# Kernel tuning notes

Hardware: AMD Instinct MI355X
Metric: run time of the kernel (lower is better)

Reference implementation:

```python
import jax, jax.numpy as jnp
import numpy as np

N, E, G = 50000, 800000, 512
DIN, HID, DOUT, L, DE = 64, 64, 128, 3, 16
NEG_SLOPE = 0.2
BN_EPS = 1e-5


def setup_inputs() -> dict:
    key = jax.random.key(0)
    ks = jax.random.split(key, 20)
    s = 0.1  # weight scale for numerical stability
    return {
        "x": jax.random.normal(ks[0], (N, DIN), jnp.float32),
        "edge_index": jax.random.randint(ks[1], (2, E), 0, N, jnp.int32),
        "edge_attr": jax.random.normal(ks[2], (E, DE), jnp.float32),
        "batch": jnp.sort(jax.random.randint(ks[3], (N,), 0, G, jnp.int32)),
        "emb_W": jax.random.normal(ks[4], (HID, DIN), jnp.float32) * s,
        "emb_b": jax.random.normal(ks[5], (HID,), jnp.float32) * s,
        "Wl": jax.random.normal(ks[6], (L, HID, HID), jnp.float32) * s,
        "bl": jax.random.normal(ks[7], (L, HID), jnp.float32) * s,
        "Wr": jax.random.normal(ks[8], (L, HID, HID), jnp.float32) * s,
        "br": jax.random.normal(ks[9], (L, HID), jnp.float32) * s,
        "We": jax.random.normal(ks[10], (L, HID, DE), jnp.float32) * s,
        "att": jax.random.normal(ks[11], (L, HID), jnp.float32) * s,
        "conv_bias": jax.random.normal(ks[12], (L, HID), jnp.float32) * s,
        "bn_gamma": jax.random.uniform(ks[13], (L, HID), jnp.float32, 0.5, 1.5),
        "bn_beta": jax.random.normal(ks[14], (L, HID), jnp.float32) * s,
        "bn_mean": jnp.zeros((L, HID), jnp.float32),
        "bn_var": jnp.ones((L, HID), jnp.float32),
        "lin_W": jax.random.normal(ks[15], (DOUT, HID), jnp.float32) * s,
        "lin_b": jax.random.normal(ks[16], (DOUT,), jnp.float32) * s,
    }


def _gatv2(h, src, dst, edge_attr, Wl, bl, Wr, br, We, att, bias):
    # GATv2Conv, heads=1, concat=False, with edge features
    xl = h @ Wl.T + bl                      # [N,C] source transform (also message value)
    xr = h @ Wr.T + br                      # [N,C] target transform
    ea = edge_attr @ We.T                   # [E,C]
    m = xl[src] + xr[dst] + ea              # [E,C]
    m = jax.nn.leaky_relu(m, NEG_SLOPE)
    alpha = m @ att                         # [E] attention logits
    amax = jax.ops.segment_max(alpha, dst, num_segments=N)
    ea_exp = jnp.exp(alpha - amax[dst])
    denom = jax.ops.segment_sum(ea_exp, dst, num_segments=N)
    alpha = ea_exp / (denom[dst] + 1e-16)
    out = jax.ops.segment_sum(alpha[:, None] * xl[src], dst, num_segments=N)
    return out + bias


def reference(x, edge_index, edge_attr, batch, emb_W, emb_b, Wl, bl, Wr, br,
              We, att, conv_bias, bn_gamma, bn_beta, bn_mean, bn_var, lin_W, lin_b):
    src, dst = edge_index[0], edge_index[1]
    h = x @ emb_W.T + emb_b
    for i in range(L):
        hc = _gatv2(h, src, dst, edge_attr, Wl[i], bl[i], Wr[i], br[i],
                    We[i], att[i], conv_bias[i])
        # BatchNorm (eval mode, running stats)
        hc = (hc - bn_mean[i]) * jax.lax.rsqrt(bn_var[i] + BN_EPS) * bn_gamma[i] + bn_beta[i]
        hc = jax.nn.gelu(hc, approximate=False)  # torch F.gelu default is exact erf
        h = h + hc                                # residual; dropout p=0 / eval -> identity
    out = h @ lin_W.T + lin_b                     # [N,DOUT]
    counts = jax.ops.segment_sum(jnp.ones((N,), out.dtype), batch, num_segments=G)
    pooled = jax.ops.segment_sum(out, batch, num_segments=G)
    return pooled / jnp.maximum(counts, 1.0)[:, None]
```

## Files before the change

### kernel.cpp

```cpp
#include <hip/hip_runtime.h>
#include <math.h>

#define NEG_SLOPE 0.2f
#define BN_EPS 1e-5f

template <int N> struct IC { static constexpr int v = N; };
template <bool B> struct BC { static constexpr bool v = B; };

typedef _Float16 half2v __attribute__((ext_vector_type(2)));
typedef _Float16 f16x8 __attribute__((ext_vector_type(8)));
typedef float f32x4v __attribute__((ext_vector_type(4)));

__device__ __forceinline__ half2v u2h(unsigned u) {
  union { unsigned u; half2v h; } c;
  c.u = u;
  return c.h;
}
__device__ __forceinline__ unsigned pkh(float lo, float hi) {
  union { half2v h; unsigned u; } c;
  c.h[0] = (_Float16)lo;
  c.h[1] = (_Float16)hi;
  return c.u;
}

#if defined(__has_builtin)
#if __has_builtin(__builtin_amdgcn_fdot2)
#define FDOT2(a, b, c) __builtin_amdgcn_fdot2((a), (b), (c), false)
#endif
#endif
#ifndef FDOT2
__device__ __forceinline__ float fdot2_sw(half2v a, half2v b, float c) {
  return c + (float)a[0] * (float)b[0] + (float)a[1] * (float)b[1];
}
#define FDOT2(a, b, c) fdot2_sw((a), (b), (c))
#endif

#if defined(__has_builtin)
#if __has_builtin(__builtin_amdgcn_exp2f)
#define FEXP(x) __builtin_amdgcn_exp2f(x)
#define ATT_SCALE 1.44269504088896f
#endif
#endif
#ifndef FEXP
#define FEXP(x) __expf(x)
#define ATT_SCALE 1.0f
#endif

#define FMA4(acc, v, wq) \
  acc += (v).x * (wq).x + (v).y * (wq).y + (v).z * (wq).z + (v).w * (wq).w

#define DOT_ROW(buf, r, bias, OUT)                                     \
  {                                                                    \
    __builtin_amdgcn_sched_barrier(0);                                 \
    float a0 = 0.f, a1 = 0.f, a2 = 0.f, a3 = 0.f;                      \
    _Pragma("unroll") for (int q = 0; q < 4; q++) {                    \
      float4 v0 = *(const float4*)((buf) + (r) * 64 + q * 16 + 0);     \
      float4 v1 = *(const float4*)((buf) + (r) * 64 + q * 16 + 4);     \
      float4 v2 = *(const float4*)((buf) + (r) * 64 + q * 16 + 8);     \
      float4 v3 = *(const float4*)((buf) + (r) * 64 + q * 16 + 12);    \
      FMA4(a0, v0, W[q * 4 + 0]);                                      \
      FMA4(a1, v1, W[q * 4 + 1]);                                      \
      FMA4(a2, v2, W[q * 4 + 2]);                                      \
      FMA4(a3, v3, W[q * 4 + 3]);                                      \
    }                                                                  \
    OUT = (bias) + ((a0 + a1) + (a2 + a3));                            \
  }

__device__ __forceinline__ float wave_sum64(float v) {
  int x;
  x = __builtin_amdgcn_update_dpp(0, __float_as_int(v), 0x121, 0xF, 0xF, true);
  v += __int_as_float(x);
  x = __builtin_amdgcn_update_dpp(0, __float_as_int(v), 0x122, 0xF, 0xF, true);
  v += __int_as_float(x);
  x = __builtin_amdgcn_update_dpp(0, __float_as_int(v), 0x124, 0xF, 0xF, true);
  v += __int_as_float(x);
  x = __builtin_amdgcn_update_dpp(0, __float_as_int(v), 0x128, 0xF, 0xF, true);
  v += __int_as_float(x);
  x = __builtin_amdgcn_update_dpp(0, __float_as_int(v), 0x142, 0xF, 0xF, true);
  v += __int_as_float(x);
  x = __builtin_amdgcn_update_dpp(0, __float_as_int(v), 0x143, 0xF, 0xF, true);
  v += __int_as_float(x);
  return __int_as_float(__builtin_amdgcn_readlane(__float_as_int(v), 63));
}

__global__ __launch_bounds__(256) void hist_kernel(
    const int* __restrict__ dst, const int* __restrict__ batch,
    int* __restrict__ deg, float* __restrict__ counts, int E_, int N_) {
  int i = blockIdx.x * 256 + threadIdx.x;
  if (i < E_) atomicAdd(&deg[dst[i]], 1);
  if (i < N_) atomicAdd(&counts[batch[i]], 1.0f);
}

__global__ __launch_bounds__(256) void scanA_kernel(
    const int* __restrict__ deg, int* __restrict__ row_ptr,
    int* __restrict__ segTot, int N_, int nseg) {
  __shared__ int sb[256];
  int t = threadIdx.x;
  for (int s = blockIdx.x; s < nseg; s += gridDim.x) {
    int i = s * 256 + t;
    int v = (i < N_) ? deg[i] : 0;
    sb[t] = v;
    __syncthreads();
    for (int off = 1; off < 256; off <<= 1) {
      int a = (t >= off) ? sb[t - off] : 0;
      __syncthreads();
      sb[t] += a;
      __syncthreads();
    }
    int incl = sb[t];
    if (i < N_) row_ptr[i] = incl - v;
    if (t == 255) segTot[s] = incl;
    __syncthreads();
  }
}

__global__ __launch_bounds__(256) void scanB_kernel(int* __restrict__ segTot,
                                                    int nseg) {
  __shared__ int sb[256];
  __shared__ int baseSh;
  int t = threadIdx.x;
  if (t == 0) baseSh = 0;
  __syncthreads();
  for (int c0 = 0; c0 < nseg; c0 += 256) {
    int s = c0 + t;
    int v = (s < nseg) ? segTot[s] : 0;
    sb[t] = v;
    __syncthreads();
    for (int off = 1; off < 256; off <<= 1) {
      int a = (t >= off) ? sb[t - off] : 0;
      __syncthreads();
      sb[t] += a;
      __syncthreads();
    }
    int incl = sb[t];
    int base = baseSh;
    if (s < nseg) segTot[s] = base + incl - v;
    __syncthreads();
    if (t == 255) baseSh = base + incl;
    __syncthreads();
  }
}

__global__ __launch_bounds__(256) void scanC_kernel(
    int* __restrict__ row_ptr, const int* __restrict__ segTot,
    int* __restrict__ cursor, int N_, int E_) {
  int tid = blockIdx.x * 256 + threadIdx.x;
  int nt = gridDim.x * 256;
  for (int i = tid; i < N_; i += nt) {
    int rp = row_ptr[i] + segTot[i >> 8];
    row_ptr[i] = rp;
    cursor[i] = rp;
  }
  if (tid == 0) row_ptr[N_] = E_;
}

__global__ __launch_bounds__(256) void dhist_kernel(
    const int* __restrict__ row_ptr, int* __restrict__ bins, int N_) {
  __shared__ int lb[128];
  int t = threadIdx.x;
  if (t < 128) lb[t] = 0;
  __syncthreads();
  int i = blockIdx.x * 256 + t;
  if (i < N_) {
    int dg = row_ptr[i + 1] - row_ptr[i];
    atomicAdd(&lb[127 - min(dg, 127)], 1);
  }
  __syncthreads();
  if (t < 128 && lb[t]) atomicAdd(&bins[t], lb[t]);
}

__global__ __launch_bounds__(128) void dscan_kernel(int* __restrict__ bins) {
  __shared__ int sb[128];
  int t = threadIdx.x;
  int v = bins[t];
  sb[t] = v;
  __syncthreads();
  for (int off = 1; off < 128; off <<= 1) {
    int a = (t >= off) ? sb[t - off] : 0;
    __syncthreads();
    sb[t] += a;
    __syncthreads();
  }
  bins[t] = sb[t] - v;
}

__global__ __launch_bounds__(256) void dscatter_kernel(
    const int* __restrict__ row_ptr, int* __restrict__ bins,
    int* __restrict__ perm, int N_) {
  __shared__ int lb[128];
  int t = threadIdx.x;
  if (t < 128) lb[t] = 0;
  __syncthreads();
  int i = blockIdx.x * 256 + t;
  int bin = 0, r = 0;
  bool ok = (i < N_);
  if (ok) {
    int dg = row_ptr[i + 1] - row_ptr[i];
    bin = 127 - min(dg, 127);
    r = atomicAdd(&lb[bin], 1);
  }
  __syncthreads();
  if (t < 128) {
    int c = lb[t];
    lb[t] = c ? atomicAdd(&bins[t], c) : 0;
  }
  __syncthreads();
  if (ok) perm[lb[bin] + r] = i;
}

__global__ __launch_bounds__(256) void scatter_kernel(
    const int* __restrict__ src, const int* __restrict__ dst,
    int* __restrict__ cursor, int* __restrict__ csr_src,
    int* __restrict__ csr_eid, int E_) {
  int e = blockIdx.x * 256 + threadIdx.x;
  if (e >= E_) return;
  int pos = atomicAdd(&cursor[dst[e]], 1);
  csr_src[pos] = src[e];
  csr_eid[pos] = e;
}

__global__ __launch_bounds__(256) void permute_attr_kernel(
    const float4* __restrict__ edge_attr4, const int* __restrict__ csr_eid,
    unsigned* __restrict__ attr_u, int E_) {
  int p = blockIdx.x * 256 + threadIdx.x;
  if (p >= E_) return;
  int e = csr_eid[p];
  float4 a0 = edge_attr4[(size_t)e * 4 + 0];
  float4 a1 = edge_attr4[(size_t)e * 4 + 1];
  float4 a2 = edge_attr4[(size_t)e * 4 + 2];
  float4 a3 = edge_attr4[(size_t)e * 4 + 3];
  uint4 u0, u1;
  u0.x = pkh(a0.x, a0.y);
  u0.y = pkh(a0.z, a0.w);
  u0.z = pkh(a1.x, a1.y);
  u0.w = pkh(a1.z, a1.w);
  u1.x = pkh(a2.x, a2.y);
  u1.y = pkh(a2.z, a2.w);
  u1.z = pkh(a3.x, a3.y);
  u1.w = pkh(a3.z, a3.w);
  uint4* d4 = (uint4*)(attr_u + (size_t)p * 8);
  d4[0] = u0;
  d4[1] = u1;
}

__global__ __launch_bounds__(256) void pack_w16_kernel(
    const float* __restrict__ Wl, const float* __restrict__ Wr,
    _Float16* __restrict__ w16, int per) {
  int i = blockIdx.x * 256 + threadIdx.x;
  if (i < per) {
    w16[i] = (_Float16)Wl[i];
  } else if (i < 2 * per) {
    w16[i] = (_Float16)Wr[i - per];
  }
}

__global__ __launch_bounds__(256, 3) void emb_kernel(
    const float* __restrict__ x, const float* __restrict__ emb_W,
    const float* __restrict__ emb_b, float* __restrict__ h, int rows) {
  __shared__ float sx[4096];
  int lane = threadIdx.x & 63;
  int w = threadIdx.x >> 6;
  int n0 = blockIdx.x * 64;

  {
    int gmax = rows * 64 - 4;
#pragma unroll
    for (int i = 0; i < 4; i++) {
      int off = w * 1024 + i * 256 + lane * 4;
      int g = min(n0 * 64 + off, gmax);
      *(float4*)(sx + off) = *(const float4*)(x + g);
    }
  }

  float4 W[16];
#pragma unroll
  for (int q = 0; q < 16; q++) W[q] = ((const float4*)(emb_W + lane * 64))[q];
  float b = emb_b[lane];
#pragma unroll 1
  for (int t = 0; t < 16; t++) {
    int r = w * 16 + t;
    float a;
    DOT_ROW(sx, r, b, a);
    int n = n0 + r;
    if (n < rows) h[(size_t)n * 64 + lane] = a;
  }
}

#if defined(__has_builtin)
#if __has_builtin(__builtin_amdgcn_mfma_f32_16x16x32_f16)
#define HAVE_MFMA16 1
#endif
#endif

__global__ __launch_bounds__(256) void linx_mfma_kernel(
    const float* __restrict__ in, const _Float16* __restrict__ Wl16,
    const float* __restrict__ bl, const _Float16* __restrict__ Wr16,
    const float* __restrict__ br, _Float16* __restrict__ xl,
    _Float16* __restrict__ xr, int rows) {
#ifdef HAVE_MFMA16
  int lane = threadIdx.x & 63;
  int w = threadIdx.x >> 6;
  int n0 = blockIdx.x * 64 + w * 16;
  int r = lane & 15;
  int kg = lane >> 4;

  int nA = min(n0 + r, rows - 1);
  f16x8 A0, A1;
  {
    const float* p = in + (size_t)nA * 64 + kg * 8;
    float4 xa = *(const float4*)(p);
    float4 xb = *(const float4*)(p + 4);
    A0[0] = (_Float16)xa.x; A0[1] = (_Float16)xa.y;
    A0[2] = (_Float16)xa.z; A0[3] = (_Float16)xa.w;
    A0[4] = (_Float16)xb.x; A0[5] = (_Float16)xb.y;
    A0[6] = (_Float16)xb.z; A0[7] = (_Float16)xb.w;
    xa = *(const float4*)(p + 32);
    xb = *(const float4*)(p + 36);
    A1[0] = (_Float16)xa.x; A1[1] = (_Float16)xa.y;
    A1[2] = (_Float16)xa.z; A1[3] = (_Float16)xa.w;
    A1[4] = (_Float16)xb.x; A1[5] = (_Float16)xb.y;
    A1[6] = (_Float16)xb.z; A1[7] = (_Float16)xb.w;
  }

#pragma unroll
  for (int c = 0; c < 4; c++) {
    int o = c * 16 + r;
    {
      const f16x8* b0 = (const f16x8*)(Wl16 + (size_t)o * 64 + kg * 8);
      const f16x8* b1 = (const f16x8*)(Wl16 + (size_t)o * 64 + 32 + kg * 8);
      f32x4v acc;
      float bv = bl[o];
      acc[0] = bv; acc[1] = bv; acc[2] = bv; acc[3] = bv;
      acc = __builtin_amdgcn_mfma_f32_16x16x32_f16(A0, b0[0], acc, 0, 0, 0);
      acc = __builtin_amdgcn_mfma_f32_16x16x32_f16(A1, b1[0], acc, 0, 0, 0);
#pragma unroll
      for (int g = 0; g < 4; g++) {
        int nd = n0 + kg * 4 + g;
        if (nd < rows) xl[(size_t)nd * 64 + o] = (_Float16)acc[g];
      }
    }
    {
      const f16x8* b0 = (const f16x8*)(Wr16 + (size_t)o * 64 + kg * 8);
      const f16x8* b1 = (const f16x8*)(Wr16 + (size_t)o * 64 + 32 + kg * 8);
      f32x4v acc;
      float bv = br[o];
      acc[0] = bv; acc[1] = bv; acc[2] = bv; acc[3] = bv;
      acc = __builtin_amdgcn_mfma_f32_16x16x32_f16(A0, b0[0], acc, 0, 0, 0);
      acc = __builtin_amdgcn_mfma_f32_16x16x32_f16(A1, b1[0], acc, 0, 0, 0);
#pragma unroll
      for (int g = 0; g < 4; g++) {
        int nd = n0 + kg * 4 + g;
        if (nd < rows) xr[(size_t)nd * 64 + o] = (_Float16)acc[g];
      }
    }
  }
#endif
}

template <bool CONTIG>
__global__ __launch_bounds__(256) void gat_fused_kernel(
    const int* __restrict__ perm, const int* __restrict__ csr_src,
    const int* __restrict__ csr_eid, const int* __restrict__ row_ptr,
    const unsigned* __restrict__ attr_u, const float* __restrict__ edge_attr,
    const _Float16* __restrict__ xl, const _Float16* __restrict__ xr,
    const float* __restrict__ We, const float* __restrict__ att,
    const float* __restrict__ conv_bias, const float* __restrict__ gamma,
    const float* __restrict__ beta, const float* __restrict__ mean,
    const float* __restrict__ var, float* __restrict__ h, int N_) {
  int widx = (blockIdx.x * 256 + threadIdx.x) >> 6;
  if (widx >= N_) return;
  int d = __builtin_amdgcn_readfirstlane(perm[widx]);
  int j = threadIdx.x & 63;
  half2v Wek2[8];
  float Wekf[16];
  if constexpr (CONTIG) {
#pragma unroll
    for (int q = 0; q < 8; q++) {
      Wek2[q][0] = (_Float16)We[j * 16 + 2 * q];
      Wek2[q][1] = (_Float16)We[j * 16 + 2 * q + 1];
    }
  } else {
#pragma unroll
    for (int k = 0; k < 16; k++) Wekf[k] = We[j * 16 + k];
  }
  float att_j = att[j] * ATT_SCALE;
  float sc = rsqrtf(var[j] + BN_EPS) * gamma[j];
  float sh = (conv_bias[j] - mean[j]) * sc + beta[j];

  int beg = __builtin_amdgcn_readfirstlane(row_ptr[d]);
  int end = __builtin_amdgcn_readfirstlane(row_ptr[d + 1]);
  float xrj = (float)xr[(size_t)d * 64 + j];
  float m = -INFINITY, l = 0.f, acc = 0.f;

  auto chunk = [&](int base, auto C_, auto PAD_) {
    constexpr int C = decltype(C_)::v;
    constexpr bool PAD = decltype(PAD_)::v;
    int si[C];
#pragma unroll
    for (int t = 0; t < C; t++) {
      int idx = PAD ? min(base + t, end - 1) : (base + t);
      si[t] = __builtin_amdgcn_readfirstlane(csr_src[idx]);
    }
    float xlv[C];
#pragma unroll
    for (int t = 0; t < C; t++)
      xlv[t] = (float)xl[(size_t)si[t] * 64 + j];
    float v[C];
#pragma unroll
    for (int t = 0; t < C; t++) {
      int idx = PAD ? min(base + t, end - 1) : (base + t);
      float ea;
      if constexpr (CONTIG) {
        const uint4* ap = (const uint4*)(attr_u + (size_t)idx * 8);
        uint4 ua = ap[0], ub = ap[1];
        ea = 0.f;
        ea = FDOT2(u2h(ua.x), Wek2[0], ea);
        ea = FDOT2(u2h(ua.y), Wek2[1], ea);
        ea = FDOT2(u2h(ua.z), Wek2[2], ea);
        ea = FDOT2(u2h(ua.w), Wek2[3], ea);
        ea = FDOT2(u2h(ub.x), Wek2[4], ea);
        ea = FDOT2(u2h(ub.y), Wek2[5], ea);
        ea = FDOT2(u2h(ub.z), Wek2[6], ea);
        ea = FDOT2(u2h(ub.w), Wek2[7], ea);
      } else {
        const float4* ap =
            (const float4*)(edge_attr + (size_t)csr_eid[idx] * 16);
        float4 a0 = ap[0], a1 = ap[1], a2 = ap[2], a3 = ap[3];
        ea = a0.x * Wekf[0]  + a0.y * Wekf[1]  + a0.z * Wekf[2]  + a0.w * Wekf[3]
           + a1.x * Wekf[4]  + a1.y * Wekf[5]  + a1.z * Wekf[6]  + a1.w * Wekf[7]
           + a2.x * Wekf[8]  + a2.y * Wekf[9]  + a2.z * Wekf[10] + a2.w * Wekf[11]
           + a3.x * Wekf[12] + a3.y * Wekf[13] + a3.z * Wekf[14] + a3.w * Wekf[15];
      }
      float z = xlv[t] + xrj + ea;
      z = fmaxf(z, NEG_SLOPE * z);
      float p = wave_sum64(z * att_j);
      v[t] = (!PAD || (base + t < end)) ? p : -INFINITY;
    }
    float mc = v[0];
#pragma unroll
    for (int t = 1; t < C; t++) mc = fmaxf(mc, v[t]);
    float newm = fmaxf(m, mc);
    float s = FEXP(m - newm);
    l *= s;
    acc *= s;
#pragma unroll
    for (int t = 0; t < C; t++) {
      float w = FEXP(v[t] - newm);
      l += w;
      acc += w * xlv[t];
    }
    m = newm;
  };

  int base = beg;
  for (; base + 16 <= end; base += 16) chunk(base, IC<16>{}, BC<false>{});
  if (base + 8 <= end) {
    chunk(base, IC<8>{}, BC<false>{});
    base += 8;
  }
  if (base + 4 <= end) {
    chunk(base, IC<4>{}, BC<false>{});
    base += 4;
  }
  if (base < end) chunk(base, IC<4>{}, BC<true>{});

  float val = acc / (l + 1e-16f) * sc + sh;
  float g = 0.5f * val * (1.f + erff(val * 0.70710678118654752f));
  h[(size_t)d * 64 + j] += g;
}

__global__ __launch_bounds__(256, 2) void lin_pool_kernel(
    const float* __restrict__ h, const float* __restrict__ lin_W,
    const float* __restrict__ lin_b, const int* __restrict__ batch,
    const float* __restrict__ counts, float* __restrict__ pooled, int rows) {
  __shared__ float shh[4096];
  int lane = threadIdx.x & 63;
  int w = threadIdx.x >> 6;
  int n0 = blockIdx.x * 64;

  {
    int gmax = rows * 64 - 4;
#pragma unroll
    for (int i = 0; i < 4; i++) {
      int off = w * 1024 + i * 256 + lane * 4;
      int g = min(n0 * 64 + off, gmax);
      *(float4*)(shh + off) = *(const float4*)(h + g);
    }
  }

  float4 W0[16], W1[16];
#pragma unroll
  for (int q = 0; q < 16; q++) W0[q] = ((const float4*)(lin_W + lane * 64))[q];
#pragma unroll
  for (int q = 0; q < 16; q++)
    W1[q] = ((const float4*)(lin_W + (lane + 64) * 64))[q];
  float b0 = lin_b[lane], b1 = lin_b[lane + 64];

  int curg = -1;
  float acc0 = 0.f, acc1 = 0.f;
  int lim = min(16, rows - n0 - w * 16);
#pragma unroll 1
  for (int t = 0; t < lim; t++) {
    int r = w * 16 + t;
    __builtin_amdgcn_sched_barrier(0);
    float d0 = b0, d1 = b1;
#pragma unroll
    for (int q = 0; q < 16; q++) {
      float4 v = *(const float4*)(shh + r * 64 + q * 4);
      FMA4(d0, v, W0[q]);
      FMA4(d1, v, W1[q]);
    }
    int g = batch[n0 + r];
    if (g != curg) {
      if (curg >= 0) {
        float inv = 1.f / fmaxf(counts[curg], 1.f);
        atomicAdd(&pooled[curg * 128 + lane], acc0 * inv);
        atomicAdd(&pooled[curg * 128 + 64 + lane], acc1 * inv);
      }
      curg = g;
      acc0 = 0.f;
      acc1 = 0.f;
    }
    acc0 += d0;
    acc1 += d1;
  }
  if (curg >= 0) {
    float inv = 1.f / fmaxf(counts[curg], 1.f);
    atomicAdd(&pooled[curg * 128 + lane], acc0 * inv);
    atomicAdd(&pooled[curg * 128 + 64 + lane], acc1 * inv);
  }
}

extern "C" void kernel_launch(void* const* d_in, const int* in_sizes, int n_in,
                              void* d_out, int out_size, void* d_ws, size_t ws_size,
                              hipStream_t stream) {
  const float* x         = (const float*)d_in[0];
  const int*   edge_index= (const int*)  d_in[1];
  const float* edge_attr = (const float*)d_in[2];
  const int*   batch     = (const int*)  d_in[3];
  const float* emb_W     = (const float*)d_in[4];
  const float* emb_b     = (const float*)d_in[5];
  const float* Wl        = (const float*)d_in[6];
  const float* bl        = (const float*)d_in[7];
  const float* Wr        = (const float*)d_in[8];
  const float* br        = (const float*)d_in[9];
  const float* We        = (const float*)d_in[10];
  const float* att       = (const float*)d_in[11];
  const float* conv_bias = (const float*)d_in[12];
  const float* bn_gamma  = (const float*)d_in[13];
  const float* bn_beta   = (const float*)d_in[14];
  const float* bn_mean   = (const float*)d_in[15];
  const float* bn_var    = (const float*)d_in[16];
  const float* lin_W     = (const float*)d_in[17];
  const float* lin_b     = (const float*)d_in[18];

  const int N_ = in_sizes[0] / 64;
  const int E_ = in_sizes[1] / 2;
  const int G_ = out_size / 128;
  const int* src = edge_index;
  const int* dst = edge_index + E_;

  const int Npad = (N_ + 3) & ~3;
  const int Epad = (E_ + 19) & ~3;
  const int nseg = (N_ + 255) / 256;

  float* ws      = (float*)d_ws;
  float* h       = ws;
  _Float16* xl   = (_Float16*)(h + (size_t)N_ * 64);
  _Float16* xr   = xl + (size_t)N_ * 64;
  int*   csr_src = (int*)(xr + (size_t)N_ * 64);
  int*   csr_eid = csr_src + Epad;
  int*   row_ptr = csr_eid + Epad;
  int*   cursor  = row_ptr + (Npad + 4);
  int*   deg     = cursor + Npad;
  float* counts  = (float*)(deg + Npad);
  int*   segTot  = (int*)(counts + G_);
  int*   bins    = segTot + nseg + 8;
  uintptr_t abp  = (uintptr_t)(bins + 128);
  abp = (abp + 15) & ~(uintptr_t)15;
  _Float16* w16  = (_Float16*)abp;
  uintptr_t abp2 = abp + 24576 * sizeof(_Float16);
  unsigned* attr_u = (unsigned*)abp2;
  int* perm = deg;

  size_t base_bytes = (abp2 - (uintptr_t)d_ws);
  bool contig = ws_size >= base_bytes + (size_t)E_ * 32 + 64;

  const int hgrid = (max(E_, N_) + 255) / 256;
  const int ngrid = (N_ + 255) / 256;
  const int egrid = (E_ + 255) / 256;

  hipMemsetAsync(deg, 0, ((size_t)Npad + G_) * 4, stream);
  hist_kernel<<<hgrid, 256, 0, stream>>>(dst, batch, deg, counts, E_, N_);
  scanA_kernel<<<min(nseg, 1024), 256, 0, stream>>>(deg, row_ptr, segTot, N_,
                                                    nseg);
  scanB_kernel<<<1, 256, 0, stream>>>(segTot, nseg);
  scanC_kernel<<<ngrid, 256, 0, stream>>>(row_ptr, segTot, cursor, N_, E_);
  scatter_kernel<<<egrid, 256, 0, stream>>>(src, dst, cursor, csr_src,
                                            csr_eid, E_);
  hipMemsetAsync(bins, 0, 128 * 4, stream);
  dhist_kernel<<<ngrid, 256, 0, stream>>>(row_ptr, bins, N_);
  dscan_kernel<<<1, 128, 0, stream>>>(bins);
  dscatter_kernel<<<ngrid, 256, 0, stream>>>(row_ptr, bins, perm, N_);
  if (contig) {
    permute_attr_kernel<<<egrid, 256, 0, stream>>>(
        (const float4*)edge_attr, csr_eid, attr_u, E_);
  }

  pack_w16_kernel<<<(24576 + 255) / 256, 256, 0, stream>>>(Wl, Wr, w16,
                                                           12288);
  const int tgrid = (N_ + 63) / 64;
  emb_kernel<<<tgrid, 256, 0, stream>>>(x, emb_W, emb_b, h, N_);

  const int gatBlocks = (N_ + 3) / 4;
  for (int l = 0; l < 3; l++) {
    linx_mfma_kernel<<<tgrid, 256, 0, stream>>>(
        h, w16 + (size_t)l * 4096, bl + l * 64, w16 + 12288 + (size_t)l * 4096,
        br + l * 64, xl, xr, N_);
    if (contig) {
      gat_fused_kernel<true><<<gatBlocks, 256, 0, stream>>>(
          perm, csr_src, csr_eid, row_ptr, attr_u, edge_attr, xl, xr,
          We + (size_t)l * 1024, att + l * 64, conv_bias + l * 64,
          bn_gamma + l * 64, bn_beta + l * 64, bn_mean + l * 64,
          bn_var + l * 64, h, N_);
    } else {
      gat_fused_kernel<false><<<gatBlocks, 256, 0, stream>>>(
          perm, csr_src, csr_eid, row_ptr, attr_u, edge_attr, xl, xr,
          We + (size_t)l * 1024, att + l * 64, conv_bias + l * 64,
          bn_gamma + l * 64, bn_beta + l * 64, bn_mean + l * 64,
          bn_var + l * 64, h, N_);
    }
  }

  hipMemsetAsync(d_out, 0, (size_t)G_ * 128 * 4, stream);
  lin_pool_kernel<<<(N_ + 63) / 64, 256, 0, stream>>>(
      h, lin_W, lin_b, batch, counts, (float*)d_out, N_);
}
```

Baseline: 571.4 us.

## Fuse preprocessing kernels and merge first-layer linear transforms into embedding

Folds the degree histogram, bin scan and degree-sorted permutation into the existing CSR scan kernels, and moves the fp16 weight packing into the histogram kernel. The embedding kernel now also computes the layer-0 xl/xr projections with MFMA from shared memory, so the first linx launch is skipped. Perm gets its own buffer instead of aliasing deg, since deg is now read after the permutation is built. This cuts kernel launches and an HBM round trip of h, at the cost of more shared memory and register pressure in the embedding kernel.

Result: faster. 543.7 us (-4.8%).

```diff
diff --git a/kernel.cpp b/kernel.cpp
--- a/kernel.cpp
+++ b/kernel.cpp
@@ -49,21 +49,21 @@
 #define FMA4(acc, v, wq) \
   acc += (v).x * (wq).x + (v).y * (wq).y + (v).z * (wq).z + (v).w * (wq).w
 
-#define DOT_ROW(buf, r, bias, OUT)                                     \
-  {                                                                    \
-    __builtin_amdgcn_sched_barrier(0);                                 \
-    float a0 = 0.f, a1 = 0.f, a2 = 0.f, a3 = 0.f;                      \
-    _Pragma("unroll") for (int q = 0; q < 4; q++) {                    \
-      float4 v0 = *(const float4*)((buf) + (r) * 64 + q * 16 + 0);     \
-      float4 v1 = *(const float4*)((buf) + (r) * 64 + q * 16 + 4);     \
-      float4 v2 = *(const float4*)((buf) + (r) * 64 + q * 16 + 8);     \
-      float4 v3 = *(const float4*)((buf) + (r) * 64 + q * 16 + 12);    \
-      FMA4(a0, v0, W[q * 4 + 0]);                                      \
-      FMA4(a1, v1, W[q * 4 + 1]);                                      \
-      FMA4(a2, v2, W[q * 4 + 2]);                                      \
-      FMA4(a3, v3, W[q * 4 + 3]);                                      \
-    }                                                                  \
-    OUT = (bias) + ((a0 + a1) + (a2 + a3));                            \
+#define DOT_ROW(buf, stride, r, bias, OUT)                                  \
+  {                                                                         \
+    __builtin_amdgcn_sched_barrier(0);                                      \
+    float a0 = 0.f, a1 = 0.f, a2 = 0.f, a3 = 0.f;                           \
+    _Pragma("unroll") for (int q = 0; q < 4; q++) {                         \
+      float4 v0 = *(const float4*)((buf) + (r) * (stride) + q * 16 + 0);    \
+      float4 v1 = *(const float4*)((buf) + (r) * (stride) + q * 16 + 4);    \
+      float4 v2 = *(const float4*)((buf) + (r) * (stride) + q * 16 + 8);    \
+      float4 v3 = *(const float4*)((buf) + (r) * (stride) + q * 16 + 12);   \
+      FMA4(a0, v0, W[q * 4 + 0]);                                           \
+      FMA4(a1, v1, W[q * 4 + 1]);                                           \
+      FMA4(a2, v2, W[q * 4 + 2]);                                           \
+      FMA4(a3, v3, W[q * 4 + 3]);                                           \
+    }                                                                       \
+    OUT = (bias) + ((a0 + a1) + (a2 + a3));                                 \
   }
 
 __device__ __forceinline__ float wave_sum64(float v) {
@@ -83,22 +83,36 @@
   return __int_as_float(__builtin_amdgcn_readlane(__float_as_int(v), 63));
 }
 
+#if defined(__has_builtin)
+#if __has_builtin(__builtin_amdgcn_mfma_f32_16x16x32_f16)
+#define HAVE_MFMA16 1
+#endif
+#endif
+
 __global__ __launch_bounds__(256) void hist_kernel(
     const int* __restrict__ dst, const int* __restrict__ batch,
-    int* __restrict__ deg, float* __restrict__ counts, int E_, int N_) {
+    int* __restrict__ deg, float* __restrict__ counts,
+    const float* __restrict__ Wl, const float* __restrict__ Wr,
+    _Float16* __restrict__ w16, int E_, int N_) {
   int i = blockIdx.x * 256 + threadIdx.x;
   if (i < E_) atomicAdd(&deg[dst[i]], 1);
   if (i < N_) atomicAdd(&counts[batch[i]], 1.0f);
+  if (i < 24576)
+    w16[i] = (i < 12288) ? (_Float16)Wl[i] : (_Float16)Wr[i - 12288];
 }
 
 __global__ __launch_bounds__(256) void scanA_kernel(
     const int* __restrict__ deg, int* __restrict__ row_ptr,
-    int* __restrict__ segTot, int N_, int nseg) {
+    int* __restrict__ segTot, int* __restrict__ bins, int N_, int nseg) {
   __shared__ int sb[256];
+  __shared__ int lb[128];
   int t = threadIdx.x;
+  if (t < 128) lb[t] = 0;
+  __syncthreads();
   for (int s = blockIdx.x; s < nseg; s += gridDim.x) {
     int i = s * 256 + t;
     int v = (i < N_) ? deg[i] : 0;
+    if (i < N_) atomicAdd(&lb[127 - min(v, 127)], 1);
     sb[t] = v;
     __syncthreads();
     for (int off = 1; off < 256; off <<= 1) {
@@ -112,9 +126,11 @@
     if (t == 255) segTot[s] = incl;
     __syncthreads();
   }
+  if (t < 128 && lb[t]) atomicAdd(&bins[t], lb[t]);
 }
 
 __global__ __launch_bounds__(256) void scanB_kernel(int* __restrict__ segTot,
+                                                    int* __restrict__ bins,
                                                     int nseg) {
   __shared__ int sb[256];
   __shared__ int baseSh;
@@ -139,73 +155,46 @@
     if (t == 255) baseSh = base + incl;
     __syncthreads();
   }
+  int v2 = (t < 128) ? bins[t] : 0;
+  sb[t] = v2;
+  __syncthreads();
+  for (int off = 1; off < 256; off <<= 1) {
+    int a = (t >= off) ? sb[t - off] : 0;
+    __syncthreads();
+    sb[t] += a;
+    __syncthreads();
+  }
+  if (t < 128) bins[t] = sb[t] - v2;
 }
 
 __global__ __launch_bounds__(256) void scanC_kernel(
     int* __restrict__ row_ptr, const int* __restrict__ segTot,
-    int* __restrict__ cursor, int N_, int E_) {
-  int tid = blockIdx.x * 256 + threadIdx.x;
-  int nt = gridDim.x * 256;
-  for (int i = tid; i < N_; i += nt) {
-    int rp = row_ptr[i] + segTot[i >> 8];
-    row_ptr[i] = rp;
-    cursor[i] = rp;
-  }
-  if (tid == 0) row_ptr[N_] = E_;
-}
-
-__global__ __launch_bounds__(256) void dhist_kernel(
-    const int* __restrict__ row_ptr, int* __restrict__ bins, int N_) {
+    int* __restrict__ cursor, const int* __restrict__ deg,
+    int* __restrict__ bins, int* __restrict__ perm, int N_, int E_) {
   __shared__ int lb[128];
+  __shared__ int lbase[128];
   int t = threadIdx.x;
   if (t < 128) lb[t] = 0;
   __syncthreads();
   int i = blockIdx.x * 256 + t;
-  if (i < N_) {
-    int dg = row_ptr[i + 1] - row_ptr[i];
-    atomicAdd(&lb[127 - min(dg, 127)], 1);
-  }
-  __syncthreads();
-  if (t < 128 && lb[t]) atomicAdd(&bins[t], lb[t]);
-}
-
-__global__ __launch_bounds__(128) void dscan_kernel(int* __restrict__ bins) {
-  __shared__ int sb[128];
-  int t = threadIdx.x;
-  int v = bins[t];
-  sb[t] = v;
-  __syncthreads();
-  for (int off = 1; off < 128; off <<= 1) {
-    int a = (t >= off) ? sb[t - off] : 0;
-    __syncthreads();
-    sb[t] += a;
-    __syncthreads();
-  }
-  bins[t] = sb[t] - v;
-}
-
-__global__ __launch_bounds__(256) void dscatter_kernel(
-    const int* __restrict__ row_ptr, int* __restrict__ bins,
-    int* __restrict__ perm, int N_) {
-  __shared__ int lb[128];
-  int t = threadIdx.x;
-  if (t < 128) lb[t] = 0;
-  __syncthreads();
-  int i = blockIdx.x * 256 + t;
-  int bin = 0, r = 0;
+  int bin = 0, rk = 0;
   bool ok = (i < N_);
   if (ok) {
-    int dg = row_ptr[i + 1] - row_ptr[i];
+    int rp = row_ptr[i] + segTot[i >> 8];
+    row_ptr[i] = rp;
+    cursor[i] = rp;
+    int dg = deg[i];
     bin = 127 - min(dg, 127);
-    r = atomicAdd(&lb[bin], 1);
-  }
+    rk = atomicAdd(&lb[bin], 1);
+  }
+  if (i == 0) row_ptr[N_] = E_;
   __syncthreads();
   if (t < 128) {
     int c = lb[t];
-    lb[t] = c ? atomicAdd(&bins[t], c) : 0;
+    lbase[t] = c ? atomicAdd(&bins[t], c) : 0;
   }
   __syncthreads();
-  if (ok) perm[lb[bin] + r] = i;
+  if (ok) perm[lbase[bin] + rk] = i;
 }
 
 __global__ __launch_bounds__(256) void scatter_kernel(
@@ -243,21 +232,14 @@
   d4[1] = u1;
 }
 
-__global__ __launch_bounds__(256) void pack_w16_kernel(
-    const float* __restrict__ Wl, const float* __restrict__ Wr,
-    _Float16* __restrict__ w16, int per) {
-  int i = blockIdx.x * 256 + threadIdx.x;
-  if (i < per) {
-    w16[i] = (_Float16)Wl[i];
-  } else if (i < 2 * per) {
-    w16[i] = (_Float16)Wr[i - per];
-  }
-}
-
 __global__ __launch_bounds__(256, 3) void emb_kernel(
     const float* __restrict__ x, const float* __restrict__ emb_W,
-    const float* __restrict__ emb_b, float* __restrict__ h, int rows) {
+    const float* __restrict__ emb_b, const _Float16* __restrict__ Wl16,
+    const float* __restrict__ bl, const _Float16* __restrict__ Wr16,
+    const float* __restrict__ br, float* __restrict__ h,
+    _Float16* __restrict__ xl, _Float16* __restrict__ xr, int rows) {
   __shared__ float sx[4096];
+  __shared__ float sh[64 * 68];
   int lane = threadIdx.x & 63;
   int w = threadIdx.x >> 6;
   int n0 = blockIdx.x * 64;
@@ -272,25 +254,78 @@
     }
   }
 
-  float4 W[16];
-#pragma unroll
-  for (int q = 0; q < 16; q++) W[q] = ((const float4*)(emb_W + lane * 64))[q];
-  float b = emb_b[lane];
+  {
+    float4 W[16];
+#pragma unroll
+    for (int q = 0; q < 16; q++) W[q] = ((const float4*)(emb_W + lane * 64))[q];
+    float b = emb_b[lane];
 #pragma unroll 1
-  for (int t = 0; t < 16; t++) {
-    int r = w * 16 + t;
-    float a;
-    DOT_ROW(sx, r, b, a);
-    int n = n0 + r;
-    if (n < rows) h[(size_t)n * 64 + lane] = a;
-  }
-}
-
-#if defined(__has_builtin)
-#if __has_builtin(__builtin_amdgcn_mfma_f32_16x16x32_f16)
-#define HAVE_MFMA16 1
-#endif
-#endif
+    for (int t = 0; t < 16; t++) {
+      int r = w * 16 + t;
+      float a;
+      DOT_ROW(sx, 64, r, b, a);
+      sh[r * 68 + lane] = a;
+      int n = n0 + r;
+      if (n < rows) h[(size_t)n * 64 + lane] = a;
+    }
+  }
+
+#ifdef HAVE_MFMA16
+  {
+    int r = lane & 15;
+    int kg = lane >> 4;
+    int nb = n0 + w * 16;
+    const float* p = sh + (w * 16 + r) * 68 + kg * 8;
+    f16x8 A0, A1;
+    {
+      float4 xa = *(const float4*)(p);
+      float4 xb = *(const float4*)(p + 4);
+      A0[0] = (_Float16)xa.x; A0[1] = (_Float16)xa.y;
+      A0[2] = (_Float16)xa.z; A0[3] = (_Float16)xa.w;
+      A0[4] = (_Float16)xb.x; A0[5] = (_Float16)xb.y;
+      A0[6] = (_Float16)xb.z; A0[7] = (_Float16)xb.w;
+      xa = *(const float4*)(p + 32);
+      xb = *(const float4*)(p + 36);
+      A1[0] = (_Float16)xa.x; A1[1] = (_Float16)xa.y;
+      A1[2] = (_Float16)xa.z; A1[3] = (_Float16)xa.w;
+      A1[4] = (_Float16)xb.x; A1[5] = (_Float16)xb.y;
+      A1[6] = (_Float16)xb.z; A1[7] = (_Float16)xb.w;
+    }
+#pragma unroll
+    for (int c = 0; c < 4; c++) {
+      int o = c * 16 + r;
+      {
+        const f16x8* b0 = (const f16x8*)(Wl16 + (size_t)o * 64 + kg * 8);
+        const f16x8* b1 = (const f16x8*)(Wl16 + (size_t)o * 64 + 32 + kg * 8);
+        f32x4v acc;
+        float bv = bl[o];
+        acc[0] = bv; acc[1] = bv; acc[2] = bv; acc[3] = bv;
+        acc = __builtin_amdgcn_mfma_f32_16x16x32_f16(A0, b0[0], acc, 0, 0, 0);
+        acc = __builtin_amdgcn_mfma_f32_16x16x32_f16(A1, b1[0], acc, 0, 0, 0);
+#pragma unroll
+        for (int g = 0; g < 4; g++) {
+          int nd = nb + kg * 4 + g;
+          if (nd < rows) xl[(size_t)nd * 64 + o] = (_Float16)acc[g];
+        }
+      }
+      {
+        const f16x8* b0 = (const f16x8*)(Wr16 + (size_t)o * 64 + kg * 8);
+        const f16x8* b1 = (const f16x8*)(Wr16 + (size_t)o * 64 + 32 + kg * 8);
+        f32x4v acc;
+        float bv = br[o];
+        acc[0] = bv; acc[1] = bv; acc[2] = bv; acc[3] = bv;
+        acc = __builtin_amdgcn_mfma_f32_16x16x32_f16(A0, b0[0], acc, 0, 0, 0);
+        acc = __builtin_amdgcn_mfma_f32_16x16x32_f16(A1, b1[0], acc, 0, 0, 0);
+#pragma unroll
+        for (int g = 0; g < 4; g++) {
+          int nd = nb + kg * 4 + g;
+          if (nd < rows) xr[(size_t)nd * 64 + o] = (_Float16)acc[g];
+        }
+      }
+    }
+  }
+#endif
+}
 
 __global__ __launch_bounds__(256) void linx_mfma_kernel(
     const float* __restrict__ in, const _Float16* __restrict__ Wl16,
@@ -576,12 +611,12 @@
   float* counts  = (float*)(deg + Npad);
   int*   segTot  = (int*)(counts + G_);
   int*   bins    = segTot + nseg + 8;
-  uintptr_t abp  = (uintptr_t)(bins + 128);
+  int*   perm    = bins + 128;
+  uintptr_t abp  = (uintptr_t)(perm + Npad);
   abp = (abp + 15) & ~(uintptr_t)15;
   _Float16* w16  = (_Float16*)abp;
   uintptr_t abp2 = abp + 24576 * sizeof(_Float16);
   unsigned* attr_u = (unsigned*)abp2;
-  int* perm = deg;
 
   size_t base_bytes = (abp2 - (uintptr_t)d_ws);
   bool contig = ws_size >= base_bytes + (size_t)E_ * 32 + 64;
@@ -590,33 +625,32 @@
   const int ngrid = (N_ + 255) / 256;
   const int egrid = (E_ + 255) / 256;
 
-  hipMemsetAsync(deg, 0, ((size_t)Npad + G_) * 4, stream);
-  hist_kernel<<<hgrid, 256, 0, stream>>>(dst, batch, deg, counts, E_, N_);
-  scanA_kernel<<<min(nseg, 1024), 256, 0, stream>>>(deg, row_ptr, segTot, N_,
-                                                    nseg);
-  scanB_kernel<<<1, 256, 0, stream>>>(segTot, nseg);
-  scanC_kernel<<<ngrid, 256, 0, stream>>>(row_ptr, segTot, cursor, N_, E_);
+  hipMemsetAsync(deg, 0, ((size_t)Npad + G_ + nseg + 8 + 128) * 4, stream);
+  hist_kernel<<<hgrid, 256, 0, stream>>>(dst, batch, deg, counts, Wl, Wr,
+                                         w16, E_, N_);
+  scanA_kernel<<<min(nseg, 1024), 256, 0, stream>>>(deg, row_ptr, segTot,
+                                                    bins, N_, nseg);
+  scanB_kernel<<<1, 256, 0, stream>>>(segTot, bins, nseg);
+  scanC_kernel<<<ngrid, 256, 0, stream>>>(row_ptr, segTot, cursor, deg, bins,
+                                          perm, N_, E_);
   scatter_kernel<<<egrid, 256, 0, stream>>>(src, dst, cursor, csr_src,
                                             csr_eid, E_);
-  hipMemsetAsync(bins, 0, 128 * 4, stream);
-  dhist_kernel<<<ngrid, 256, 0, stream>>>(row_ptr, bins, N_);
-  dscan_kernel<<<1, 128, 0, stream>>>(bins);
-  dscatter_kernel<<<ngrid, 256, 0, stream>>>(row_ptr, bins, perm, N_);
   if (contig) {
     permute_attr_kernel<<<egrid, 256, 0, stream>>>(
         (const float4*)edge_attr, csr_eid, attr_u, E_);
   }
 
-  pack_w16_kernel<<<(24576 + 255) / 256, 256, 0, stream>>>(Wl, Wr, w16,
-                                                           12288);
   const int tgrid = (N_ + 63) / 64;
-  emb_kernel<<<tgrid, 256, 0, stream>>>(x, emb_W, emb_b, h, N_);
+  emb_kernel<<<tgrid, 256, 0, stream>>>(x, emb_W, emb_b, w16, bl,
+                                        w16 + 12288, br, h, xl, xr, N_);
 
   const int gatBlocks = (N_ + 3) / 4;
   for (int l = 0; l < 3; l++) {
-    linx_mfma_kernel<<<tgrid, 256, 0, stream>>>(
-        h, w16 + (size_t)l * 4096, bl + l * 64, w16 + 12288 + (size_t)l * 4096,
-        br + l * 64, xl, xr, N_);
+    if (l > 0) {
+      linx_mfma_kernel<<<tgrid, 256, 0, stream>>>(
+          h, w16 + (size_t)l * 4096, bl + l * 64,
+          w16 + 12288 + (size_t)l * 4096, br + l * 64, xl, xr, N_);
+    }
     if (contig) {
       gat_fused_kernel<true><<<gatBlocks, 256, 0, stream>>>(
           perm, csr_src, csr_eid, row_ptr, attr_u, edge_attr, xl, xr,
```
